# Optimization experiments

Hardware: AMD Instinct MI355X
Metric: run time of the kernel (lower is better)

The kernel has to match this reference:

```python
import jax, jax.numpy as jnp
import numpy as np
from jax import lax

B, S, C, D, V = 256, 50, 40, 256, 20000
T_DIFF = 1000
BETA_START, BETA_END = 1e-4, 2e-2


def _lstm(x, Wih, Whh, bih, bhh):
    # x: [B,S,D]; single-layer LSTM, batch_first, eval mode (no dropout)
    Bb = x.shape[0]
    H = Whh.shape[1]
    def step(carry, xt):
        h, c = carry
        g = xt @ Wih.T + bih + h @ Whh.T + bhh  # [B,4H]
        i, f, gg, o = jnp.split(g, 4, axis=-1)
        i = jax.nn.sigmoid(i); f = jax.nn.sigmoid(f)
        gg = jnp.tanh(gg); o = jax.nn.sigmoid(o)
        c = f * c + i * gg
        h = o * jnp.tanh(c)
        return (h, c), h
    h0 = jnp.zeros((Bb, H), x.dtype)
    (_, _), hs = lax.scan(step, (h0, h0), x.transpose(1, 0, 2))
    return hs.transpose(1, 0, 2)  # [B,S,H]


def setup_inputs() -> dict:
    key = jax.random.key(0)
    ks = jax.random.split(key, 20)
    sc = 0.05
    inp = {
        'input_seqs': jax.random.randint(ks[0], (B, S, C), 0, V),
        'masks': jnp.zeros((B, S), jnp.int32),
        'lengths': jax.random.randint(ks[1], (B,), 1, S + 1),
        'seq_time_step': jax.random.uniform(ks[2], (B, S), jnp.float32),
        'code_masks': jnp.zeros((B, S, C), jnp.int32),
        'diffusion_time_t': jax.random.randint(ks[3], (B,), 0, T_DIFF),
        'normal_noise': jax.random.normal(ks[4], (B, S, D), jnp.float32),
        # learned parameters
        'emb': jax.random.normal(ks[5], (V + 1, D), jnp.float32) * sc,
        'Wih': jax.random.normal(ks[6], (4 * D, D), jnp.float32) * sc,
        'Whh': jax.random.normal(ks[7], (4 * D, D), jnp.float32) * sc,
        'bih': jnp.zeros((4 * D,), jnp.float32),
        'bhh': jnp.zeros((4 * D,), jnp.float32),
        'Whk': jax.random.normal(ks[8], (D, D), jnp.float32) * sc,
        'bhk': jnp.zeros((D,), jnp.float32),
        'W1': jax.random.normal(ks[9], (64, 2 * D), jnp.float32) * sc,
        'b1': jnp.zeros((64,), jnp.float32),
        'W2': jax.random.normal(ks[10], (2, 64), jnp.float32) * sc,
        'b2': jnp.zeros((2,), jnp.float32),
        'Wdiff': jax.random.normal(ks[11], (D, D), jnp.float32) * sc,
        'bdiff': jnp.zeros((D,), jnp.float32),
        'temb': jax.random.normal(ks[12], (T_DIFF, D), jnp.float32) * sc,
        'Wout': jax.random.normal(ks[13], (2, D), jnp.float32) * sc,
        'bout': jnp.zeros((2,), jnp.float32),
    }
    # padding_idx row zeroed like nn.Embedding(padding_idx=-1)
    inp['emb'] = inp['emb'].at[V].set(0.0)
    return inp


def reference(input_seqs, masks, lengths, seq_time_step, code_masks,
              diffusion_time_t, normal_noise,
              emb, Wih, Whh, bih, bhh, Whk, bhk, W1, b1, W2, b2,
              Wdiff, bdiff, temb, Wout, bout):
    # embedding sum over codes per visit
    x = emb[input_seqs].sum(axis=2)  # [B,S,D]
    rnn_out = _lstm(x, Wih, Whh, bih, bhh)  # [B,S,D]

    # vectorized alignment loop: e_k is ALWAYS x[:,0] (as in source),
    # position i>=1 attends between e_k and w_hk(rnn_out[i-1])
    w = rnn_out @ Whk.T + bhk  # [B,S,D]
    e_k = x[:, :1, :]  # [B,1,D]
    wprev = w[:, :-1, :]  # [B,S-1,D] -> timestep i uses w[i-1]
    cat = jnp.concatenate([jnp.broadcast_to(e_k, wprev.shape), wprev], -1)
    attn = jax.nn.softmax(jnp.tanh(cat @ W1.T + b1) @ W2.T + b2, axis=-1)  # [B,S-1,2]
    aligned_rest = e_k * attn[..., 0:1] + wprev * attn[..., 1:2]
    aligned_e_t = jnp.concatenate([e_k, aligned_rest], axis=1)  # [B,S,D]

    # diffusion noising (linear beta schedule as in ehr.yml defaults)
    betas = jnp.linspace(BETA_START, BETA_END, T_DIFF, dtype=jnp.float32)
    alpha = jnp.cumprod(1.0 - betas)[diffusion_time_t][:, None, None]
    noisy = aligned_e_t * jnp.sqrt(alpha) + normal_noise * jnp.sqrt(1.0 - alpha)

    # UNet surrogate (source unavailable): timestep-conditioned linear map
    predicted_noise = (noisy + temb[diffusion_time_t][:, None, :]) @ Wdiff + bdiff

    gen_x = aligned_e_t + (normal_noise - predicted_noise)
    pool_x = jnp.max(x, axis=1) @ Wout.T + bout  # [B,2]
    gen_pool_x = jnp.max(gen_x, axis=1) @ Wout.T + bout  # [B,2]
    return (pool_x, gen_pool_x, predicted_noise, normal_noise)
```

## Files before the change

### kernel.cpp

```cpp
#include <hip/hip_runtime.h>
#include <cmath>

#define Bb 256
#define Ss 50
#define Cc 40
#define Dd 256
#define Vv 20000

typedef __bf16 bf16;
typedef __bf16 bf16x8 __attribute__((ext_vector_type(8)));
typedef float f32x4 __attribute__((ext_vector_type(4)));
typedef unsigned long long u64;

#define GL2LDS(g, l) __builtin_amdgcn_global_load_lds( \
    (__attribute__((address_space(1))) void*)(g), \
    (__attribute__((address_space(3))) void*)(l), 16, 0, 0)

#define OFFB_GATES    0ull
#define OFFB_WBB      13107200ull
#define OFFB_H1       32505856ull
#define OFFB_X        52428800ull
#define OFFB_XB       65536000ull
#define OFFB_RNNB     72089600ull
#define OFFB_W        78643200ull
#define OFFB_BAR      91750400ull
#define OFFB_WIHB     92012544ull
#define OFFB_WHHB     92536832ull
#define OFFB_WHKB     93061120ull
#define OFFB_W1B      93192192ull
#define OFFB_WDTB     93257728ull
#define OFFB_SALPHA   93388800ull
#define OFFB_SBETA    93389824ull

template<int BM, int BN, int ACT>
__global__ __launch_bounds__(256) void mfma_gemm(
    const bf16* __restrict__ A, int lda,
    const bf16* __restrict__ B, int ldb,
    const float* __restrict__ bias1, const float* __restrict__ bias2,
    float* __restrict__ C, bf16* __restrict__ Cb, int ldc, int K)
{
    constexpr int BK = 32;
    constexpr int NF = BN / 32;
    __shared__ bf16 As[BM * BK];
    __shared__ bf16 Bs[BN * BK];
    const int tid  = threadIdx.x;
    const int wave = tid >> 6;
    const int lane = tid & 63;
    const int m0 = blockIdx.x * BM;
    const int n0 = blockIdx.y * BN;
    const int wm = (wave >> 1) * 64;
    const int wn = (wave & 1) * (BN / 2);

    f32x4 acc[4][NF];
#pragma unroll
    for (int i = 0; i < 4; ++i)
#pragma unroll
        for (int j = 0; j < NF; ++j) acc[i][j] = (f32x4){0.f, 0.f, 0.f, 0.f};

    const int ar = tid >> 2;
    const int ac = tid & 3;
    const int sw = ac ^ (ar & 3);
    const int lr = lane & 15;
    const int q  = lane >> 4;

    for (int k0 = 0; k0 < K; k0 += BK) {
        __syncthreads();
#pragma unroll
        for (int it = 0; it < BM / 64; ++it) {
            const bf16* gp = A + (size_t)(m0 + it * 64 + ar) * lda + k0 + sw * 8;
            GL2LDS(gp, As + it * 2048 + wave * 512);
        }
#pragma unroll
        for (int it = 0; it < BN / 64; ++it) {
            const bf16* gp = B + (size_t)(n0 + it * 64 + ar) * ldb + k0 + sw * 8;
            GL2LDS(gp, Bs + it * 2048 + wave * 512);
        }
        __syncthreads();

        bf16x8 af[4], bfv[NF];
#pragma unroll
        for (int fm = 0; fm < 4; ++fm) {
            int m = wm + fm * 16 + lr;
            af[fm] = *(const bf16x8*)(As + m * 32 + ((q ^ (m & 3)) * 8));
        }
#pragma unroll
        for (int fn = 0; fn < NF; ++fn) {
            int n = wn + fn * 16 + lr;
            bfv[fn] = *(const bf16x8*)(Bs + n * 32 + ((q ^ (n & 3)) * 8));
        }
#pragma unroll
        for (int fm = 0; fm < 4; ++fm)
#pragma unroll
            for (int fn = 0; fn < NF; ++fn)
                acc[fm][fn] = __builtin_amdgcn_mfma_f32_16x16x32_bf16(
                    af[fm], bfv[fn], acc[fm][fn], 0, 0, 0);
    }

    const int rbase = q * 4;
#pragma unroll
    for (int fn = 0; fn < NF; ++fn) {
        const int col = n0 + wn + fn * 16 + lr;
        float bb = 0.f;
        if (bias1) bb += bias1[col];
        if (bias2) bb += bias2[col];
#pragma unroll
        for (int fm = 0; fm < 4; ++fm) {
            f32x4 v = acc[fm][fn];
#pragma unroll
            for (int r = 0; r < 4; ++r) {
                const int row = m0 + wm + fm * 16 + rbase + r;
                float val = v[r] + bb;
                if (ACT == 1) val = tanhf(val);
                C[(size_t)row * ldc + col] = val;
                if (Cb) Cb[(size_t)row * ldc + col] = (bf16)val;
            }
        }
    }
}

__global__ __launch_bounds__(256) void h1_gemm(
    const bf16* __restrict__ xb, const bf16* __restrict__ wbb,
    const bf16* __restrict__ W1b,
    const float* __restrict__ b1, float* __restrict__ H1)
{
    constexpr int BM = 128, BN = 64, BK = 32, NF = 2;
    constexpr int K = 512;
    __shared__ bf16 As[BM * BK];
    __shared__ bf16 Bs[BN * BK];
    const int tid  = threadIdx.x;
    const int wave = tid >> 6;
    const int lane = tid & 63;
    const int m0 = blockIdx.x * BM;
    const int wm = (wave >> 1) * 64;
    const int wn = (wave & 1) * 32;

    f32x4 acc[4][NF];
#pragma unroll
    for (int i = 0; i < 4; ++i)
#pragma unroll
        for (int j = 0; j < NF; ++j) acc[i][j] = (f32x4){0.f, 0.f, 0.f, 0.f};

    const int ar = tid >> 2;
    const int ac = tid & 3;
    const int sw = ac ^ (ar & 3);
    const int lr = lane & 15;
    const int q  = lane >> 4;

    for (int k0 = 0; k0 < K; k0 += BK) {
        __syncthreads();
#pragma unroll
        for (int it = 0; it < 2; ++it) {
            const int row = m0 + it * 64 + ar;
            const int b = row / (Ss - 1), t = row - b * (Ss - 1);
            const int col = k0 + sw * 8;
            const bf16* gp = (col < 256)
                ? xb  + (size_t)b * (Ss * Dd) + col
                : wbb + ((size_t)(b * Ss + t)) * Dd + (col - 256);
            GL2LDS(gp, As + it * 2048 + wave * 512);
        }
        {
            const bf16* gp = W1b + (size_t)ar * K + k0 + sw * 8;
            GL2LDS(gp, Bs + wave * 512);
        }
        __syncthreads();

        bf16x8 af[4], bfv[NF];
#pragma unroll
        for (int fm = 0; fm < 4; ++fm) {
            int m = wm + fm * 16 + lr;
            af[fm] = *(const bf16x8*)(As + m * 32 + ((q ^ (m & 3)) * 8));
        }
#pragma unroll
        for (int fn = 0; fn < NF; ++fn) {
            int n = wn + fn * 16 + lr;
            bfv[fn] = *(const bf16x8*)(Bs + n * 32 + ((q ^ (n & 3)) * 8));
        }
#pragma unroll
        for (int fm = 0; fm < 4; ++fm)
#pragma unroll
            for (int fn = 0; fn < NF; ++fn)
                acc[fm][fn] = __builtin_amdgcn_mfma_f32_16x16x32_bf16(
                    af[fm], bfv[fn], acc[fm][fn], 0, 0, 0);
    }

    const int rbase = q * 4;
#pragma unroll
    for (int fn = 0; fn < NF; ++fn) {
        const int col = wn + fn * 16 + lr;
        const float bb = b1[col];
#pragma unroll
        for (int fm = 0; fm < 4; ++fm) {
            f32x4 v = acc[fm][fn];
#pragma unroll
            for (int r = 0; r < 4; ++r) {
                const int row = m0 + wm + fm * 16 + rbase + r;
                H1[(size_t)row * 64 + col] = tanhf(v[r] + bb);
            }
        }
    }
}

__global__ __launch_bounds__(512, 2) void lstm_quad(
    const bf16* __restrict__ Whhb,
    const float* __restrict__ gates,
    bf16* __restrict__ rnnb,
    unsigned* __restrict__ bar,
    const float* __restrict__ xf,
    const float* __restrict__ Wout, const float* __restrict__ bout,
    float* __restrict__ outp)
{
    if (blockIdx.x >= 64) {
        __shared__ float r0[4], r1[4];
        const int b = blockIdx.x - 64;
        const int tid = threadIdx.x;
        if (tid < 256) {
            float m = -INFINITY;
            for (int s = 0; s < Ss; ++s)
                m = fmaxf(m, xf[((size_t)b * Ss + s) * Dd + tid]);
            float v0 = m * Wout[tid];
            float v1 = m * Wout[Dd + tid];
#pragma unroll
            for (int off = 32; off; off >>= 1) {
                v0 += __shfl_down(v0, off);
                v1 += __shfl_down(v1, off);
            }
            if ((tid & 63) == 0) { r0[tid >> 6] = v0; r1[tid >> 6] = v1; }
        }
        __syncthreads();
        if (tid == 0) {
            outp[b * 2 + 0] = r0[0] + r0[1] + r0[2] + r0[3] + bout[0];
            outp[b * 2 + 1] = r1[0] + r1[1] + r1[2] + r1[3] + bout[1];
        }
        return;
    }

    __shared__ bf16 hb0[16 * 256];
    __shared__ bf16 hb1[16 * 256];
    __shared__ float pacc[4][4][16][17];
    const int tid  = threadIdx.x;
    const int w    = tid >> 6;
    const int lane = tid & 63;
    const int lr   = lane & 15;
    const int q    = lane >> 4;
    const int bm   = blockIdx.x & 15;
    const int bd   = blockIdx.x >> 4;
    const int kh   = w >> 2;
    const int ct   = w & 3;
    const int dg   = bd * 64 + ct * 16 + lr;

    f32x4 wfr[4][4];
#pragma unroll
    for (int g = 0; g < 4; ++g) {
        const bf16* brow = Whhb + (size_t)(g * 256 + dg) * Dd + kh * 128 + q * 8;
#pragma unroll
        for (int kc = 0; kc < 4; ++kc)
            wfr[g][kc] = *(const f32x4*)(brow + kc * 32);
    }

    const float* gp[4];
#pragma unroll
    for (int r = 0; r < 4; ++r)
        gp[r] = gates + (size_t)(bm * 16 + q * 4 + r) * (Ss * 1024) + dg;

    const int xrow = tid >> 4, xc8 = tid & 15;
    const size_t my_base = ((size_t)(bm * 16 + xrow) * Ss) * Dd + bd * 64 + xc8 * 4;
    const int pack_off = xrow * 512 + (((bd * 8 + (xc8 >> 1)) ^ (xrow & 7)) << 4) + (xc8 & 1) * 8;

    const int pA  = tid >> 8;
    const int pdA = pA + (pA >= bd ? 1 : 0);
    const int pdB = 2 + (2 >= bd ? 1 : 0);
    const int rowA = (tid >> 4) & 15, xqA = tid & 15;
    const size_t gA = ((size_t)(bm * 16 + rowA) * Ss) * Dd + pdA * 64 + xqA * 4;
    const size_t gB = ((size_t)(bm * 16 + xrow) * Ss) * Dd + pdB * 64 + xc8 * 4;
    const int unpA = rowA * 512 + (((pdA * 8 + (xqA >> 1)) ^ (rowA & 7)) << 4) + (xqA & 1) * 8;
    const int unpB = xrow * 512 + (((pdB * 8 + (xc8 >> 1)) ^ (xrow & 7)) << 4) + (xc8 & 1) * 8;
    unsigned* myf = bar + (bm * 4 + bd) * 32;
    unsigned* pfA = bar + (bm * 4 + pdA) * 32;
    unsigned* pfB = bar + (bm * 4 + pdB) * 32;

    int ew_off[4];
#pragma unroll
    for (int r = 0; r < 4; ++r) {
        const int row = q * 4 + r;
        ew_off[r] = row * 512 + (((dg >> 3) ^ (row & 7)) << 4) + (dg & 7) * 2;
    }

    float c[4] = {0.f, 0.f, 0.f, 0.f};
    float gaA[4][4], gaB[4][4];
    if (kh == 0) {
#pragma unroll
        for (int r = 0; r < 4; ++r)
#pragma unroll
            for (int g = 0; g < 4; ++g) gaA[g][r] = gp[r][g * 256];
    }

#define STEP(T, GACUR, GANEXT, RD, WR, FIRST)                                   \
    {                                                                           \
        f32x4 acc[4];                                                           \
        _Pragma("unroll")                                                       \
        for (int g = 0; g < 4; ++g) acc[g] = (f32x4){0.f, 0.f, 0.f, 0.f};       \
        if (!(FIRST)) {                                                         \
            bf16x8 af[4];                                                       \
            _Pragma("unroll")                                                   \
            for (int kc = 0; kc < 4; ++kc)                                      \
                af[kc] = *(const bf16x8*)((const char*)(RD) + lr * 512          \
                         + (((kh * 16 + kc * 4 + q) ^ (lr & 7)) << 4));         \
            _Pragma("unroll")                                                   \
            for (int kc = 0; kc < 4; ++kc)                                      \
                _Pragma("unroll")                                               \
                for (int g = 0; g < 4; ++g)                                     \
                    acc[g] = __builtin_amdgcn_mfma_f32_16x16x32_bf16(           \
                        af[kc], __builtin_bit_cast(bf16x8, wfr[g][kc]),         \
                        acc[g], 0, 0, 0);                                       \
        }                                                                       \
        if (kh == 1) {                                                          \
            _Pragma("unroll")                                                   \
            for (int g = 0; g < 4; ++g)                                         \
                _Pragma("unroll")                                               \
                for (int r = 0; r < 4; ++r)                                     \
                    pacc[ct][g][q * 4 + r][lr] = acc[g][r];                     \
        }                                                                       \
        __syncthreads();                          \
        if (kh == 0) {                                                          \
            _Pragma("unroll")                                                   \
            for (int r = 0; r < 4; ++r) {                                       \
                float gi = acc[0][r] + pacc[ct][0][q * 4 + r][lr] + GACUR[0][r];\
                float gf = acc[1][r] + pacc[ct][1][q * 4 + r][lr] + GACUR[1][r];\
                float gg = acc[2][r] + pacc[ct][2][q * 4 + r][lr] + GACUR[2][r];\
                float go = acc[3][r] + pacc[ct][3][q * 4 + r][lr] + GACUR[3][r];\
                float ii  = 1.f / (1.f + expf(-gi));                            \
                float ff  = 1.f / (1.f + expf(-gf));                            \
                float g2t = tanhf(gg);                                          \
                float oo  = 1.f / (1.f + expf(-go));                            \
                c[r] = ff * c[r] + ii * g2t;                                    \
                *(bf16*)((char*)(WR) + ew_off[r]) = (bf16)(oo * tanhf(c[r]));   \
            }                                                                   \
        }                                                                       \
        __syncthreads();                          \
        if (tid < 256) {                                                        \
            u64 v = *(const u64*)((const char*)(WR) + pack_off);                \
            __hip_atomic_store((u64*)(rnnb + my_base + (size_t)(T) * Dd), v,    \
                               __ATOMIC_RELAXED, __HIP_MEMORY_SCOPE_AGENT);     \
        }                                                                       \
        if ((T) != Ss - 1) {                                                    \
            __syncthreads();        \
            if (tid == 0)                                                       \
                __hip_atomic_store(myf, (unsigned)((T) + 1),                    \
                                   __ATOMIC_RELAXED, __HIP_MEMORY_SCOPE_AGENT); \
            if (kh == 0) {            \
                _Pragma("unroll")                                               \
                for (int r = 0; r < 4; ++r)                                     \
                    _Pragma("unroll")                                           \
                    for (int g = 0; g < 4; ++g)                                 \
                        GANEXT[g][r] = gp[r][(size_t)((T) + 1) * 1024 + g * 256];\
            }                                                                   \
            while (__hip_atomic_load(pfA, __ATOMIC_RELAXED,                     \
                                     __HIP_MEMORY_SCOPE_AGENT)                  \
                   < (unsigned)((T) + 1)) {}                                    \
            {                                                                   \
                u64 rv = __hip_atomic_load(                                     \
                    (const u64*)(rnnb + gA + (size_t)(T) * Dd),                 \
                    __ATOMIC_RELAXED, __HIP_MEMORY_SCOPE_AGENT);                \
                *(u64*)((char*)(WR) + unpA) = rv;                               \
            }                                                                   \
            if (tid < 256) {                                                    \
                while (__hip_atomic_load(pfB, __ATOMIC_RELAXED,                 \
                                         __HIP_MEMORY_SCOPE_AGENT)              \
                       < (unsigned)((T) + 1)) {}                                \
                u64 rv = __hip_atomic_load(                                     \
                    (const u64*)(rnnb + gB + (size_t)(T) * Dd),                 \
                    __ATOMIC_RELAXED, __HIP_MEMORY_SCOPE_AGENT);                \
                *(u64*)((char*)(WR) + unpB) = rv;                               \
            }                                                                   \
            __syncthreads();           \
        }                                                                       \
    }

    for (int t2 = 0; t2 < Ss; t2 += 2) {
        STEP(t2,     gaA, gaB, hb1, hb0, (t2 == 0));
        STEP(t2 + 1, gaB, gaA, hb0, hb1, false);
    }
#undef STEP
}

__global__ __launch_bounds__(256) void prep_kernel(
    const float* __restrict__ Wih, bf16* __restrict__ Wihb,
    const float* __restrict__ Whh, bf16* __restrict__ Whhb,
    const float* __restrict__ Whk, bf16* __restrict__ Whkb,
    const float* __restrict__ W1,  bf16* __restrict__ W1b,
    const float* __restrict__ Wdiff, bf16* __restrict__ WdTb,
    const int* __restrict__ tdiff, float* __restrict__ salpha,
    float* __restrict__ sbeta, unsigned* __restrict__ bar,
    const int* __restrict__ seqs, const float* __restrict__ emb,
    float* __restrict__ x, bf16* __restrict__ xb)
{
    __shared__ float t[32][33];
    __shared__ int idx[4][Cc];
    int bx = blockIdx.x;
    const int tid = threadIdx.x;
    if (bx < 1024) { int i = bx * 256 + tid; Wihb[i] = (bf16)Wih[i]; return; }
    bx -= 1024;
    if (bx < 1024) { int i = bx * 256 + tid; Whhb[i] = (bf16)Whh[i]; return; }
    bx -= 1024;
    if (bx < 256)  { int i = bx * 256 + tid; Whkb[i] = (bf16)Whk[i]; return; }
    bx -= 256;
    if (bx < 128)  { int i = bx * 256 + tid; W1b[i]  = (bf16)W1[i];  return; }
    bx -= 128;
    if (bx < 64) {
        const int c0 = (bx & 7) * 32, r0 = (bx >> 3) * 32;
        const int tx = tid & 31, ty = tid >> 5;
        for (int i = ty; i < 32; i += 8)
            t[i][tx] = Wdiff[(size_t)(r0 + i) * 256 + c0 + tx];
        __syncthreads();
        for (int i = ty; i < 32; i += 8)
            WdTb[(size_t)(c0 + i) * 256 + r0 + tx] = (bf16)t[tx][i];
        return;
    }
    bx -= 64;
    if (bx == 0) {
#pragma unroll
        for (int j = 0; j < 8; ++j) bar[tid * 8 + j] = 0u;
        const int tt = tdiff[tid];
        const float step = (0.02f - 1e-4f) / 999.f;
        float prod = 1.f;
        for (int j = 0; j <= tt; ++j) prod *= (1.f - (1e-4f + j * step));
        salpha[tid] = sqrtf(prod);
        sbeta[tid]  = sqrtf(fmaxf(1.f - prod, 0.f));
        return;
    }
    bx -= 1;
    const int w = tid >> 6, l = tid & 63;
    const int bs0 = bx * 4;
    if (tid < 4 * Cc) idx[tid / Cc][tid % Cc] = seqs[(size_t)bs0 * Cc + tid];
    __syncthreads();
    f32x4 s = (f32x4){0.f, 0.f, 0.f, 0.f};
#pragma unroll 8
    for (int c = 0; c < Cc; ++c)
        s += *(const f32x4*)(emb + (size_t)idx[w][c] * Dd + l * 4);
    const size_t o = (size_t)(bs0 + w) * Dd + l * 4;
    *(f32x4*)(x + o) = s;
    bf16 b4[4] = {(bf16)s[0], (bf16)s[1], (bf16)s[2], (bf16)s[3]};
    *(u64*)(xb + o) = *(const u64*)b4;
}

__global__ __launch_bounds__(256) void tail_kernel(
    const float* __restrict__ x, const float* __restrict__ wbuf,
    const float* __restrict__ H1, const float* __restrict__ W2,
    const float* __restrict__ b2, const float* __restrict__ noise,
    const float* __restrict__ temb, const int* __restrict__ tdiff,
    const float* __restrict__ salpha, const float* __restrict__ sbeta,
    const bf16* __restrict__ WdTb, const float* __restrict__ bdiff,
    const float* __restrict__ Wout, const float* __restrict__ bout,
    float* __restrict__ pred_out, float* __restrict__ noise_out,
    float* __restrict__ outp_gen)
{
    __shared__ float alignedL[Ss * 256];
    __shared__ bf16  tmpbL[64 * 256];
    __shared__ bf16  Bs[256 * 32];
    __shared__ float saL[Ss - 1][2];
    __shared__ float rr0[4], rr1[4];

    const int b    = blockIdx.x;
    const int tid  = threadIdx.x;
    const int wave = tid >> 6;
    const int lane = tid & 63;
    const int lr   = lane & 15;
    const int q    = lane >> 4;

    for (int t = wave; t < Ss - 1; t += 4) {
        const int r = b * (Ss - 1) + t;
        float h = H1[(size_t)r * 64 + lane];
        float v0 = h * W2[lane];
        float v1 = h * W2[64 + lane];
#pragma unroll
        for (int off = 32; off; off >>= 1) { v0 += __shfl_down(v0, off); v1 += __shfl_down(v1, off); }
        if (lane == 0) {
            float z0 = v0 + b2[0], z1 = v1 + b2[1];
            float m = fmaxf(z0, z1);
            float e0 = expf(z0 - m), e1 = expf(z1 - m);
            float inv = 1.f / (e0 + e1);
            saL[t][0] = e0 * inv;
            saL[t][1] = e1 * inv;
        }
    }
    __syncthreads();

    {
        const int d = tid;
        const float ek = x[((size_t)b * Ss) * Dd + d];
        const int tt = tdiff[b];
        const float sa_ = salpha[b], sb_ = sbeta[b];
        const float te = temb[(size_t)tt * Dd + d];
        for (int s = 0; s < Ss; ++s) {
            float v;
            if (s == 0) v = ek;
            else v = ek * saL[s - 1][0]
                   + wbuf[((size_t)b * Ss + s - 1) * Dd + d] * saL[s - 1][1];
            alignedL[s * 256 + d] = v;
            const size_t i = ((size_t)b * Ss + s) * Dd + d;
            const float nz = noise[i];
            noise_out[i] = nz;
            const int off = s * 512 + (((d >> 3) ^ (s & 7)) << 4) + (d & 7) * 2;
            *(bf16*)((char*)tmpbL + off) = (bf16)(v * sa_ + nz * sb_ + te);
        }
#pragma unroll
        for (int s = Ss; s < 64; ++s) {
            const int off = s * 512 + (((d >> 3) ^ (s & 7)) << 4) + (d & 7) * 2;
            *(bf16*)((char*)tmpbL + off) = (bf16)0.f;
        }
    }

    f32x4 acc[4][4];
#pragma unroll
    for (int i = 0; i < 4; ++i)
#pragma unroll
        for (int j = 0; j < 4; ++j) acc[i][j] = (f32x4){0.f, 0.f, 0.f, 0.f};

    const int ar = tid >> 2, ac = tid & 3, sw = ac ^ (ar & 3);
    const int wn = wave * 64;

    for (int k0 = 0; k0 < 256; k0 += 32) {
        __syncthreads();
#pragma unroll
        for (int it = 0; it < 4; ++it) {
            const bf16* gp2 = WdTb + (size_t)(it * 64 + ar) * 256 + k0 + sw * 8;
            GL2LDS(gp2, Bs + it * 2048 + wave * 512);
        }
        __syncthreads();
        bf16x8 af[4], bfv[4];
#pragma unroll
        for (int fm = 0; fm < 4; ++fm) {
            const int m = fm * 16 + lr;
            af[fm] = *(const bf16x8*)((const char*)tmpbL + m * 512
                      + ((((k0 >> 3) + q) ^ (m & 7)) << 4));
        }
#pragma unroll
        for (int fn = 0; fn < 4; ++fn) {
            const int n = wn + fn * 16 + lr;
            bfv[fn] = *(const bf16x8*)(Bs + n * 32 + ((q ^ (n & 3)) * 8));
        }
#pragma unroll
        for (int fm = 0; fm < 4; ++fm)
#pragma unroll
            for (int fn = 0; fn < 4; ++fn)
                acc[fm][fn] = __builtin_amdgcn_mfma_f32_16x16x32_bf16(
                    af[fm], bfv[fn], acc[fm][fn], 0, 0, 0);
    }

    float v0 = 0.f, v1 = 0.f;
#pragma unroll
    for (int fn = 0; fn < 4; ++fn) {
        const int col = wn + fn * 16 + lr;
        const float bd_ = bdiff[col];
        float mx = -INFINITY;
#pragma unroll
        for (int fm = 0; fm < 4; ++fm) {
#pragma unroll
            for (int r = 0; r < 4; ++r) {
                const int row = fm * 16 + q * 4 + r;
                if (row < Ss) {
                    const float pred = acc[fm][fn][r] + bd_;
                    const size_t i = ((size_t)b * Ss + row) * Dd + col;
                    pred_out[i] = pred;
                    const float gen = alignedL[row * 256 + col] + noise[i] - pred;
                    mx = fmaxf(mx, gen);
                }
            }
        }
        mx = fmaxf(mx, __shfl_xor(mx, 16));
        mx = fmaxf(mx, __shfl_xor(mx, 32));
        if (q == 0) { v0 += mx * Wout[col]; v1 += mx * Wout[Dd + col]; }
    }
#pragma unroll
    for (int off = 32; off; off >>= 1) { v0 += __shfl_down(v0, off); v1 += __shfl_down(v1, off); }
    if (lane == 0) { rr0[wave] = v0; rr1[wave] = v1; }
    __syncthreads();
    if (tid == 0) {
        outp_gen[b * 2 + 0] = rr0[0] + rr0[1] + rr0[2] + rr0[3] + bout[0];
        outp_gen[b * 2 + 1] = rr1[0] + rr1[1] + rr1[2] + rr1[3] + bout[1];
    }
}

extern "C" void kernel_launch(void* const* d_in, const int* in_sizes, int n_in,
                              void* d_out, int out_size, void* d_ws, size_t ws_size,
                              hipStream_t stream)
{
    const int*   seqs  = (const int*)d_in[0];
    const int*   tdiff = (const int*)d_in[5];
    const float* noise = (const float*)d_in[6];
    const float* emb   = (const float*)d_in[7];
    const float* Wih   = (const float*)d_in[8];
    const float* Whh   = (const float*)d_in[9];
    const float* bih   = (const float*)d_in[10];
    const float* bhh   = (const float*)d_in[11];
    const float* Whk   = (const float*)d_in[12];
    const float* bhk   = (const float*)d_in[13];
    const float* W1    = (const float*)d_in[14];
    const float* b1    = (const float*)d_in[15];
    const float* W2    = (const float*)d_in[16];
    const float* b2    = (const float*)d_in[17];
    const float* Wdiff = (const float*)d_in[18];
    const float* bdiff = (const float*)d_in[19];
    const float* temb  = (const float*)d_in[20];
    const float* Wout  = (const float*)d_in[21];
    const float* bout  = (const float*)d_in[22];

    float* outp = (float*)d_out;
    char*  wsb  = (char*)d_ws;

    float* gates   = (float*)(wsb + OFFB_GATES);
    bf16*  wbb     = (bf16*) (wsb + OFFB_WBB);
    float* H1      = (float*)(wsb + OFFB_H1);
    float* x       = (float*)(wsb + OFFB_X);
    bf16*  xb      = (bf16*) (wsb + OFFB_XB);
    bf16*  rnnb    = (bf16*) (wsb + OFFB_RNNB);
    float* wbuf    = (float*)(wsb + OFFB_W);
    unsigned* bar  = (unsigned*)(wsb + OFFB_BAR);
    bf16*  Wihb    = (bf16*) (wsb + OFFB_WIHB);
    bf16*  Whhb    = (bf16*) (wsb + OFFB_WHHB);
    bf16*  Whkb    = (bf16*) (wsb + OFFB_WHKB);
    bf16*  W1b     = (bf16*) (wsb + OFFB_W1B);
    bf16*  WdTb    = (bf16*) (wsb + OFFB_WDTB);
    float* salpha  = (float*)(wsb + OFFB_SALPHA);
    float* sbeta   = (float*)(wsb + OFFB_SBETA);

    float* pred_out  = outp + 1024;
    float* noise_out = outp + 1024 + (size_t)Bb * Ss * Dd;

    prep_kernel<<<5697, 256, 0, stream>>>(Wih, Wihb, Whh, Whhb, Whk, Whkb,
                                          W1, W1b, Wdiff, WdTb,
                                          tdiff, salpha, sbeta, bar,
                                          seqs, emb, x, xb);

    mfma_gemm<128, 128, 0><<<dim3(100, 8), 256, 0, stream>>>(
        xb, 256, Wihb, 256, bih, bhh, gates, nullptr, 1024, 256);

    lstm_quad<<<64 + Bb, 512, 0, stream>>>(Whhb, gates, rnnb, bar,
                                           x, Wout, bout, outp);

    mfma_gemm<128, 128, 0><<<dim3(100, 2), 256, 0, stream>>>(
        rnnb, 256, Whkb, 256, bhk, nullptr, wbuf, wbb, 256, 256);

    h1_gemm<<<dim3(98, 1), 256, 0, stream>>>(xb, wbb, W1b, b1, H1);

    tail_kernel<<<Bb, 256, 0, stream>>>(
        x, wbuf, H1, W2, b2, noise, temb, tdiff, salpha, sbeta,
        WdTb, bdiff, Wout, bout, pred_out, noise_out, outp + 512);
}
```

Baseline: 423.4 us.

## Fuse Whk projection and attention MLP GEMMs into per-batch tail kernel

Removes the separate Whk GEMM and h1_gemm launches and computes w = rnn_out·Whk^T, the concatenated attention input, the tanh MLP and the softmax weights inside the per-batch tail kernel, using LDS staging. This drops two kernel launches and the global round trips for wbuf, wbb and H1. In exchange, each of the 256 blocks recomputes its 64-row GEMMs with padded rows, and the LDS arena of about 137 KB limits each CU to a single block.

```diff
diff --git a/kernel.cpp b/kernel.cpp
--- a/kernel.cpp
+++ b/kernel.cpp
@@ -17,12 +17,9 @@
     (__attribute__((address_space(3))) void*)(l), 16, 0, 0)
 
 #define OFFB_GATES    0ull
-#define OFFB_WBB      13107200ull
-#define OFFB_H1       32505856ull
 #define OFFB_X        52428800ull
 #define OFFB_XB       65536000ull
 #define OFFB_RNNB     72089600ull
-#define OFFB_W        78643200ull
 #define OFFB_BAR      91750400ull
 #define OFFB_WIHB     92012544ull
 #define OFFB_WHHB     92536832ull
@@ -37,7 +34,7 @@
     const bf16* __restrict__ A, int lda,
     const bf16* __restrict__ B, int ldb,
     const float* __restrict__ bias1, const float* __restrict__ bias2,
-    float* __restrict__ C, bf16* __restrict__ Cb, int ldc, int K)
+    float* __restrict__ C, int ldc, int K)
 {
     constexpr int BK = 32;
     constexpr int NF = BN / 32;
@@ -112,89 +109,6 @@
                 float val = v[r] + bb;
                 if (ACT == 1) val = tanhf(val);
                 C[(size_t)row * ldc + col] = val;
-                if (Cb) Cb[(size_t)row * ldc + col] = (bf16)val;
-            }
-        }
-    }
-}
-
-__global__ __launch_bounds__(256) void h1_gemm(
-    const bf16* __restrict__ xb, const bf16* __restrict__ wbb,
-    const bf16* __restrict__ W1b,
-    const float* __restrict__ b1, float* __restrict__ H1)
-{
-    constexpr int BM = 128, BN = 64, BK = 32, NF = 2;
-    constexpr int K = 512;
-    __shared__ bf16 As[BM * BK];
-    __shared__ bf16 Bs[BN * BK];
-    const int tid  = threadIdx.x;
-    const int wave = tid >> 6;
-    const int lane = tid & 63;
-    const int m0 = blockIdx.x * BM;
-    const int wm = (wave >> 1) * 64;
-    const int wn = (wave & 1) * 32;
-
-    f32x4 acc[4][NF];
-#pragma unroll
-    for (int i = 0; i < 4; ++i)
-#pragma unroll
-        for (int j = 0; j < NF; ++j) acc[i][j] = (f32x4){0.f, 0.f, 0.f, 0.f};
-
-    const int ar = tid >> 2;
-    const int ac = tid & 3;
-    const int sw = ac ^ (ar & 3);
-    const int lr = lane & 15;
-    const int q  = lane >> 4;
-
-    for (int k0 = 0; k0 < K; k0 += BK) {
-        __syncthreads();
-#pragma unroll
-        for (int it = 0; it < 2; ++it) {
-            const int row = m0 + it * 64 + ar;
-            const int b = row / (Ss - 1), t = row - b * (Ss - 1);
-            const int col = k0 + sw * 8;
-            const bf16* gp = (col < 256)
-                ? xb  + (size_t)b * (Ss * Dd) + col
-                : wbb + ((size_t)(b * Ss + t)) * Dd + (col - 256);
-            GL2LDS(gp, As + it * 2048 + wave * 512);
-        }
-        {
-            const bf16* gp = W1b + (size_t)ar * K + k0 + sw * 8;
-            GL2LDS(gp, Bs + wave * 512);
-        }
-        __syncthreads();
-
-        bf16x8 af[4], bfv[NF];
-#pragma unroll
-        for (int fm = 0; fm < 4; ++fm) {
-            int m = wm + fm * 16 + lr;
-            af[fm] = *(const bf16x8*)(As + m * 32 + ((q ^ (m & 3)) * 8));
-        }
-#pragma unroll
-        for (int fn = 0; fn < NF; ++fn) {
-            int n = wn + fn * 16 + lr;
-            bfv[fn] = *(const bf16x8*)(Bs + n * 32 + ((q ^ (n & 3)) * 8));
-        }
-#pragma unroll
-        for (int fm = 0; fm < 4; ++fm)
-#pragma unroll
-            for (int fn = 0; fn < NF; ++fn)
-                acc[fm][fn] = __builtin_amdgcn_mfma_f32_16x16x32_bf16(
-                    af[fm], bfv[fn], acc[fm][fn], 0, 0, 0);
-    }
-
-    const int rbase = q * 4;
-#pragma unroll
-    for (int fn = 0; fn < NF; ++fn) {
-        const int col = wn + fn * 16 + lr;
-        const float bb = b1[col];
-#pragma unroll
-        for (int fm = 0; fm < 4; ++fm) {
-            f32x4 v = acc[fm][fn];
-#pragma unroll
-            for (int r = 0; r < 4; ++r) {
-                const int row = m0 + wm + fm * 16 + rbase + r;
-                H1[(size_t)row * 64 + col] = tanhf(v[r] + bb);
             }
         }
     }
@@ -443,22 +357,31 @@
     *(u64*)(xb + o) = *(const u64*)b4;
 }
 
-__global__ __launch_bounds__(256) void tail_kernel(
-    const float* __restrict__ x, const float* __restrict__ wbuf,
-    const float* __restrict__ H1, const float* __restrict__ W2,
-    const float* __restrict__ b2, const float* __restrict__ noise,
-    const float* __restrict__ temb, const int* __restrict__ tdiff,
+__global__ __launch_bounds__(256) void tail2_kernel(
+    const float* __restrict__ x, const bf16* __restrict__ xb,
+    const bf16* __restrict__ rnnb,
+    const bf16* __restrict__ Whkb, const float* __restrict__ bhk,
+    const bf16* __restrict__ W1b, const float* __restrict__ b1,
+    const float* __restrict__ W2, const float* __restrict__ b2,
+    const float* __restrict__ noise, const float* __restrict__ temb,
+    const int* __restrict__ tdiff,
     const float* __restrict__ salpha, const float* __restrict__ sbeta,
     const bf16* __restrict__ WdTb, const float* __restrict__ bdiff,
     const float* __restrict__ Wout, const float* __restrict__ bout,
     float* __restrict__ pred_out, float* __restrict__ noise_out,
     float* __restrict__ outp_gen)
 {
-    __shared__ float alignedL[Ss * 256];
-    __shared__ bf16  tmpbL[64 * 256];
-    __shared__ bf16  Bs[256 * 32];
-    __shared__ float saL[Ss - 1][2];
-    __shared__ float rr0[4], rr1[4];
+    __shared__ __align__(16) char arena[139712];
+    bf16*  catL = (bf16*)(arena);
+    float* wL   = (float*)(arena + 65536);
+    bf16*  Bs   = (bf16*)(arena + 116736);
+    bf16*  As   = (bf16*)(arena + 133120);
+    float* v0L  = (float*)(arena + 137216);
+    float* v1L  = (float*)(arena + 138240);
+    float* saL  = (float*)(arena + 139264);
+    float* rr   = (float*)(arena + 139664);
+    float* alignedL = (float*)(arena);
+    bf16*  tmpbL    = (bf16*)(arena + 65536);
 
     const int b    = blockIdx.x;
     const int tid  = threadIdx.x;
@@ -466,46 +389,155 @@
     const int lane = tid & 63;
     const int lr   = lane & 15;
     const int q    = lane >> 4;
-
-    for (int t = wave; t < Ss - 1; t += 4) {
-        const int r = b * (Ss - 1) + t;
-        float h = H1[(size_t)r * 64 + lane];
-        float v0 = h * W2[lane];
-        float v1 = h * W2[64 + lane];
-#pragma unroll
-        for (int off = 32; off; off >>= 1) { v0 += __shfl_down(v0, off); v1 += __shfl_down(v1, off); }
-        if (lane == 0) {
-            float z0 = v0 + b2[0], z1 = v1 + b2[1];
-            float m = fmaxf(z0, z1);
-            float e0 = expf(z0 - m), e1 = expf(z1 - m);
-            float inv = 1.f / (e0 + e1);
-            saL[t][0] = e0 * inv;
-            saL[t][1] = e1 * inv;
+    const int ar   = tid >> 2, ac = tid & 3, sw = ac ^ (ar & 3);
+
+    const float ek  = x[((size_t)b * Ss) * Dd + tid];
+    const bf16  xbv = xb[((size_t)b * Ss) * Dd + tid];
+
+    {
+        const int chunk = tid >> 3;
+        for (int t = 0; t < 64; ++t) {
+            const int off = t * 1024 + ((chunk ^ (t & 7)) << 4) + (tid & 7) * 2;
+            *(bf16*)((char*)catL + off) = xbv;
+        }
+    }
+
+    {
+        f32x4 acc[4][4];
+#pragma unroll
+        for (int i = 0; i < 4; ++i)
+#pragma unroll
+            for (int j = 0; j < 4; ++j) acc[i][j] = (f32x4){0.f, 0.f, 0.f, 0.f};
+        const int wn = wave * 64;
+        for (int k0 = 0; k0 < 256; k0 += 32) {
+            __syncthreads();
+            GL2LDS(rnnb + ((size_t)b * Ss + ar) * Dd + k0 + sw * 8, As + wave * 512);
+#pragma unroll
+            for (int it = 0; it < 4; ++it)
+                GL2LDS(Whkb + (size_t)(it * 64 + ar) * Dd + k0 + sw * 8,
+                       Bs + it * 2048 + wave * 512);
+            __syncthreads();
+            bf16x8 af[4], bfv[4];
+#pragma unroll
+            for (int fm = 0; fm < 4; ++fm) {
+                const int m = fm * 16 + lr;
+                af[fm] = *(const bf16x8*)(As + m * 32 + ((q ^ (m & 3)) * 8));
+            }
+#pragma unroll
+            for (int fn = 0; fn < 4; ++fn) {
+                const int n = wn + fn * 16 + lr;
+                bfv[fn] = *(const bf16x8*)(Bs + n * 32 + ((q ^ (n & 3)) * 8));
+            }
+#pragma unroll
+            for (int fm = 0; fm < 4; ++fm)
+#pragma unroll
+                for (int fn = 0; fn < 4; ++fn)
+                    acc[fm][fn] = __builtin_amdgcn_mfma_f32_16x16x32_bf16(
+                        af[fm], bfv[fn], acc[fm][fn], 0, 0, 0);
+        }
+#pragma unroll
+        for (int fn = 0; fn < 4; ++fn) {
+            const int col = wn + fn * 16 + lr;
+            const float bb = bhk[col];
+#pragma unroll
+            for (int fm = 0; fm < 4; ++fm) {
+#pragma unroll
+                for (int r = 0; r < 4; ++r) {
+                    const int row = fm * 16 + q * 4 + r;
+                    const float val = acc[fm][fn][r] + bb;
+                    if (row < Ss) wL[row * 256 + col] = val;
+                    if (row < Ss - 1) {
+                        const int chunk = 32 + (col >> 3);
+                        const int off = row * 1024 + ((chunk ^ (row & 7)) << 4)
+                                        + (col & 7) * 2;
+                        *(bf16*)((char*)catL + off) = (bf16)val;
+                    }
+                }
+            }
+        }
+    }
+
+    {
+        f32x4 acc2[4];
+#pragma unroll
+        for (int i = 0; i < 4; ++i) acc2[i] = (f32x4){0.f, 0.f, 0.f, 0.f};
+        const int wn = wave * 16;
+        for (int k0 = 0; k0 < 512; k0 += 32) {
+            __syncthreads();
+            GL2LDS(W1b + (size_t)ar * 512 + k0 + sw * 8, Bs + wave * 512);
+            __syncthreads();
+            bf16x8 af2[4], bv;
+#pragma unroll
+            for (int fm = 0; fm < 4; ++fm) {
+                const int m = fm * 16 + lr;
+                const int off = m * 1024 + ((((k0 >> 3) + q) ^ (m & 7)) << 4);
+                af2[fm] = *(const bf16x8*)((const char*)catL + off);
+            }
+            {
+                const int n = wn + lr;
+                bv = *(const bf16x8*)(Bs + n * 32 + ((q ^ (n & 3)) * 8));
+            }
+#pragma unroll
+            for (int fm = 0; fm < 4; ++fm)
+                acc2[fm] = __builtin_amdgcn_mfma_f32_16x16x32_bf16(
+                    af2[fm], bv, acc2[fm], 0, 0, 0);
+        }
+        const int col = wn + lr;
+        const float b1c = b1[col];
+        const float w20 = W2[col], w21 = W2[64 + col];
+#pragma unroll
+        for (int fm = 0; fm < 4; ++fm) {
+#pragma unroll
+            for (int r = 0; r < 4; ++r) {
+                const int row = fm * 16 + q * 4 + r;
+                const float h = tanhf(acc2[fm][r] + b1c);
+                float t0 = h * w20, t1 = h * w21;
+#pragma unroll
+                for (int off = 8; off; off >>= 1) {
+                    t0 += __shfl_xor(t0, off);
+                    t1 += __shfl_xor(t1, off);
+                }
+                if (lr == 0) { v0L[row * 4 + wave] = t0; v1L[row * 4 + wave] = t1; }
+            }
         }
     }
     __syncthreads();
+    if (tid < Ss - 1) {
+        const float z0 = v0L[tid * 4] + v0L[tid * 4 + 1] + v0L[tid * 4 + 2]
+                       + v0L[tid * 4 + 3] + b2[0];
+        const float z1 = v1L[tid * 4] + v1L[tid * 4 + 1] + v1L[tid * 4 + 2]
+                       + v1L[tid * 4 + 3] + b2[1];
+        const float m = fmaxf(z0, z1);
+        const float e0 = expf(z0 - m), e1 = expf(z1 - m);
+        const float inv = 1.f / (e0 + e1);
+        saL[tid * 2 + 0] = e0 * inv;
+        saL[tid * 2 + 1] = e1 * inv;
+    }
+    __syncthreads();
+
+    for (int s = 0; s < Ss; ++s) {
+        float v;
+        if (s == 0) v = ek;
+        else v = ek * saL[(s - 1) * 2] + wL[(s - 1) * 256 + tid] * saL[(s - 1) * 2 + 1];
+        alignedL[s * 256 + tid] = v;
+        const size_t i = ((size_t)b * Ss + s) * Dd + tid;
+        noise_out[i] = noise[i];
+    }
+    __syncthreads();
 
     {
-        const int d = tid;
-        const float ek = x[((size_t)b * Ss) * Dd + d];
         const int tt = tdiff[b];
         const float sa_ = salpha[b], sb_ = sbeta[b];
-        const float te = temb[(size_t)tt * Dd + d];
+        const float te = temb[(size_t)tt * Dd + tid];
         for (int s = 0; s < Ss; ++s) {
-            float v;
-            if (s == 0) v = ek;
-            else v = ek * saL[s - 1][0]
-                   + wbuf[((size_t)b * Ss + s - 1) * Dd + d] * saL[s - 1][1];
-            alignedL[s * 256 + d] = v;
-            const size_t i = ((size_t)b * Ss + s) * Dd + d;
-            const float nz = noise[i];
-            noise_out[i] = nz;
-            const int off = s * 512 + (((d >> 3) ^ (s & 7)) << 4) + (d & 7) * 2;
-            *(bf16*)((char*)tmpbL + off) = (bf16)(v * sa_ + nz * sb_ + te);
+            const size_t i = ((size_t)b * Ss + s) * Dd + tid;
+            const float v = alignedL[s * 256 + tid];
+            const int off = s * 512 + (((tid >> 3) ^ (s & 7)) << 4) + (tid & 7) * 2;
+            *(bf16*)((char*)tmpbL + off) = (bf16)(v * sa_ + noise[i] * sb_ + te);
         }
 #pragma unroll
         for (int s = Ss; s < 64; ++s) {
-            const int off = s * 512 + (((d >> 3) ^ (s & 7)) << 4) + (d & 7) * 2;
+            const int off = s * 512 + (((tid >> 3) ^ (s & 7)) << 4) + (tid & 7) * 2;
             *(bf16*)((char*)tmpbL + off) = (bf16)0.f;
         }
     }
@@ -515,17 +547,13 @@
     for (int i = 0; i < 4; ++i)
 #pragma unroll
         for (int j = 0; j < 4; ++j) acc[i][j] = (f32x4){0.f, 0.f, 0.f, 0.f};
-
-    const int ar = tid >> 2, ac = tid & 3, sw = ac ^ (ar & 3);
     const int wn = wave * 64;
-
     for (int k0 = 0; k0 < 256; k0 += 32) {
         __syncthreads();
 #pragma unroll
-        for (int it = 0; it < 4; ++it) {
-            const bf16* gp2 = WdTb + (size_t)(it * 64 + ar) * 256 + k0 + sw * 8;
-            GL2LDS(gp2, Bs + it * 2048 + wave * 512);
-        }
+        for (int it = 0; it < 4; ++it)
+            GL2LDS(WdTb + (size_t)(it * 64 + ar) * 256 + k0 + sw * 8,
+                   Bs + it * 2048 + wave * 512);
         __syncthreads();
         bf16x8 af[4], bfv[4];
 #pragma unroll
@@ -573,11 +601,11 @@
     }
 #pragma unroll
     for (int off = 32; off; off >>= 1) { v0 += __shfl_down(v0, off); v1 += __shfl_down(v1, off); }
-    if (lane == 0) { rr0[wave] = v0; rr1[wave] = v1; }
+    if (lane == 0) { rr[wave] = v0; rr[4 + wave] = v1; }
     __syncthreads();
     if (tid == 0) {
-        outp_gen[b * 2 + 0] = rr0[0] + rr0[1] + rr0[2] + rr0[3] + bout[0];
-        outp_gen[b * 2 + 1] = rr1[0] + rr1[1] + rr1[2] + rr1[3] + bout[1];
+        outp_gen[b * 2 + 0] = rr[0] + rr[1] + rr[2] + rr[3] + bout[0];
+        outp_gen[b * 2 + 1] = rr[4] + rr[5] + rr[6] + rr[7] + bout[1];
     }
 }
 
@@ -609,12 +637,9 @@
     char*  wsb  = (char*)d_ws;
 
     float* gates   = (float*)(wsb + OFFB_GATES);
-    bf16*  wbb     = (bf16*) (wsb + OFFB_WBB);
-    float* H1      = (float*)(wsb + OFFB_H1);
     float* x       = (float*)(wsb + OFFB_X);
     bf16*  xb      = (bf16*) (wsb + OFFB_XB);
     bf16*  rnnb    = (bf16*) (wsb + OFFB_RNNB);
-    float* wbuf    = (float*)(wsb + OFFB_W);
     unsigned* bar  = (unsigned*)(wsb + OFFB_BAR);
     bf16*  Wihb    = (bf16*) (wsb + OFFB_WIHB);
     bf16*  Whhb    = (bf16*) (wsb + OFFB_WHHB);
@@ -633,17 +658,13 @@
                                           seqs, emb, x, xb);
 
     mfma_gemm<128, 128, 0><<<dim3(100, 8), 256, 0, stream>>>(
-        xb, 256, Wihb, 256, bih, bhh, gates, nullptr, 1024, 256);
+        xb, 256, Wihb, 256, bih, bhh, gates, 1024, 256);
 
     lstm_quad<<<64 + Bb, 512, 0, stream>>>(Whhb, gates, rnnb, bar,
                                            x, Wout, bout, outp);
 
-    mfma_gemm<128, 128, 0><<<dim3(100, 2), 256, 0, stream>>>(
-        rnnb, 256, Whkb, 256, bhk, nullptr, wbuf, wbb, 256, 256);
-
-    h1_gemm<<<dim3(98, 1), 256, 0, stream>>>(xb, wbb, W1b, b1, H1);
-
-    tail_kernel<<<Bb, 256, 0, stream>>>(
-        x, wbuf, H1, W2, b2, noise, temb, tdiff, salpha, sbeta,
+    tail2_kernel<<<Bb, 256, 0, stream>>>(
+        x, xb, rnnb, Whkb, bhk, W1b, b1, W2, b2,
+        noise, temb, tdiff, salpha, sbeta,
         WdTb, bdiff, Wout, bout, pred_out, noise_out, outp + 512);
 }
```

After: 404.2 us. 4.5% less time.
